# Optimization experiments

Measured on AMD Instinct MI355X. Metric: run time of the kernel, lower is better.

The kernel has to match this reference:

```python
import jax, jax.numpy as jnp
import numpy as np

HIDDEN = 2048
NUM_HEADS = 32
NUM_KV_HEADS = 8
HEAD_DIM = 128
EPS = 1e-6
ROPE_BASE = 10000.0
T = 2048


def setup_inputs() -> dict:
    key = jax.random.key(0)
    k1, k2, k3, k4, k5 = jax.random.split(key, 5)
    q_size = NUM_HEADS * HEAD_DIM
    kv_size = NUM_KV_HEADS * HEAD_DIM
    s = 0.02
    return {
        "positions": jnp.arange(T, dtype=jnp.int32),
        "hidden_states": jax.random.normal(k1, (T, HIDDEN), dtype=jnp.float32),
        "wqkv": jax.random.normal(k2, (q_size + 2 * kv_size, HIDDEN), dtype=jnp.float32) * s,
        "wo": jax.random.normal(k3, (HIDDEN, q_size), dtype=jnp.float32) * s,
        "q_norm_w": jnp.ones((HEAD_DIM,), dtype=jnp.float32),
        "k_norm_w": jnp.ones((HEAD_DIM,), dtype=jnp.float32),
    }


def _rms_norm(x, w, eps=EPS):
    # x: [T, H, D]; normalize over last dim
    var = jnp.mean(jnp.square(x), axis=-1, keepdims=True)
    return x * jax.lax.rsqrt(var + eps) * w


def _rope(positions, x):
    # neox-style rotate-half RoPE. x: [T, H, D]
    half = HEAD_DIM // 2
    inv_freq = 1.0 / (ROPE_BASE ** (jnp.arange(0, half, dtype=jnp.float32) / half))
    ang = positions.astype(jnp.float32)[:, None] * inv_freq  # [T, half]
    cos = jnp.cos(ang)[:, None, :]  # [T, 1, half]
    sin = jnp.sin(ang)[:, None, :]
    x1, x2 = x[..., :half], x[..., half:]
    return jnp.concatenate([x1 * cos - x2 * sin, x2 * cos + x1 * sin], axis=-1)


def reference(positions, hidden_states, wqkv, wo, q_norm_w, k_norm_w):
    q_size = NUM_HEADS * HEAD_DIM
    kv_size = NUM_KV_HEADS * HEAD_DIM
    scaling = HEAD_DIM ** -0.5

    qkv = hidden_states @ wqkv.T  # [T, q_size + 2*kv_size]
    q = qkv[:, :q_size].reshape(-1, NUM_HEADS, HEAD_DIM)
    k = qkv[:, q_size:q_size + kv_size].reshape(-1, NUM_KV_HEADS, HEAD_DIM)
    v = qkv[:, q_size + kv_size:].reshape(-1, NUM_KV_HEADS, HEAD_DIM)

    q = _rms_norm(q, q_norm_w)
    k = _rms_norm(k, k_norm_w)
    q = _rope(positions, q)
    k = _rope(positions, k)

    # GQA: repeat kv heads to match query heads
    group = NUM_HEADS // NUM_KV_HEADS
    k = jnp.repeat(k, group, axis=1)  # [T, H, D]
    v = jnp.repeat(v, group, axis=1)

    scores = jnp.einsum("thd,shd->hts", q, k) * scaling  # [H, T, T]
    causal = positions[:, None] >= positions[None, :]  # [T, T]
    scores = jnp.where(causal[None], scores, jnp.finfo(scores.dtype).min)
    probs = jax.nn.softmax(scores, axis=-1)
    o = jnp.einsum("hts,shd->thd", probs, v)  # [T, H, D]
    return o.reshape(-1, q_size) @ wo.T  # [T, HIDDEN]
```

## Files before the change

### kernel.cpp

```cpp
#include <hip/hip_runtime.h>
#include <hip/hip_bf16.h>

#define T_SEQ   2048
#define HIDDEN  2048
#define NUM_H   32
#define NUM_KV  8
#define HD      128
#define Q_SIZE  4096
#define QKV_N   6144

typedef __bf16 bf16;
typedef __bf16 bf16x8 __attribute__((ext_vector_type(8)));
typedef __bf16 bf16x4 __attribute__((ext_vector_type(4)));
typedef float  floatx4 __attribute__((ext_vector_type(4)));

#define GLOBAL_AS(p) ((const __attribute__((address_space(1))) void*)(p))
#define LDS_AS(p)    ((__attribute__((address_space(3))) void*)(p))

__global__ void detect_dtype(const unsigned short* __restrict__ wq, int* flagp)
{
    const int lane = threadIdx.x;
    int cnt = 0;
    for (int i = lane; i < 512; i += 64) {
        int ef = (wq[i] >> 7) & 0xFF;
        if (ef >= 90 && ef <= 130) cnt++;
    }
    #pragma unroll
    for (int m = 32; m; m >>= 1) cnt += __shfl_xor(cnt, m);
    if (lane == 0) *flagp = (cnt >= 430) ? 1 : 0;
}

__global__ __launch_bounds__(256) void convert_all(
    const void* __restrict__ h, const void* __restrict__ wq,
    const void* __restrict__ wo_, const void* __restrict__ qn,
    const void* __restrict__ kn,
    bf16* __restrict__ hb, bf16* __restrict__ wqb, bf16* __restrict__ wob,
    bf16* __restrict__ qnb, bf16* __restrict__ knb, const int* flagp)
{
    long e = ((long)blockIdx.x * 256 + threadIdx.x) * 8;
    const void* src; bf16* dst; long off;
    if      (e < 4194304)  { src = h;   dst = hb;  off = e; }
    else if (e < 16777216) { src = wq;  dst = wqb; off = e - 4194304; }
    else if (e < 25165824) { src = wo_; dst = wob; off = e - 16777216; }
    else if (e < 25165952) { src = qn;  dst = qnb; off = e - 25165824; }
    else if (e < 25166080) { src = kn;  dst = knb; off = e - 25165952; }
    else return;

    if (*flagp) {
        *(bf16x8*)(dst + off) = *(const bf16x8*)((const bf16*)src + off);
    } else {
        const float* f = (const float*)src + off;
        bf16x8 v;
        #pragma unroll
        for (int i = 0; i < 8; ++i) v[i] = (bf16)f[i];
        *(bf16x8*)(dst + off) = v;
    }
}

__global__ __launch_bounds__(256) void gemm_bt(
    const bf16* __restrict__ A, const bf16* __restrict__ B,
    void* __restrict__ Cv, int M, int N, int K, int lda,
    const int* flagp, int is_final)
{
    __shared__ bf16 As[128 * 32];
    __shared__ bf16 Bs[128 * 32];

    const int tid  = threadIdx.x;
    const int wave = tid >> 6, lane = tid & 63;
    const int quad = lane >> 4, l16 = lane & 15;
    const int wm = (wave & 1) * 64, wn = (wave >> 1) * 64;
    const long baseM = (long)blockIdx.x * 128;
    const long baseN = (long)blockIdx.y * 128;
    const int  bf_out = is_final ? *flagp : 1;

    const int  srow = wave * 16 + (lane >> 2);
    const int  scol = (lane & 3) * 8;
    const long aoff0 = (baseM + srow) * (long)lda + scol;
    const long aoff1 = (baseM + 64 + srow) * (long)lda + scol;
    const long boff0 = (baseN + srow) * (long)K + scol;
    const long boff1 = (baseN + 64 + srow) * (long)K + scol;
    const int  lds0 = wave * 512;
    const int  lds1 = 2048 + wave * 512;

    floatx4 acc[4][4] = {};

    for (int k0 = 0; k0 < K; k0 += 32) {
        __builtin_amdgcn_global_load_lds(GLOBAL_AS(A + aoff0 + k0), LDS_AS(As + lds0), 16, 0, 0);
        __builtin_amdgcn_global_load_lds(GLOBAL_AS(A + aoff1 + k0), LDS_AS(As + lds1), 16, 0, 0);
        __builtin_amdgcn_global_load_lds(GLOBAL_AS(B + boff0 + k0), LDS_AS(Bs + lds0), 16, 0, 0);
        __builtin_amdgcn_global_load_lds(GLOBAL_AS(B + boff1 + k0), LDS_AS(Bs + lds1), 16, 0, 0);
        __syncthreads();

        bf16x8 af[4], bfr[4];
        #pragma unroll
        for (int i = 0; i < 4; ++i)
            af[i] = *(const bf16x8*)(As + (wm + i * 16 + l16) * 32 + quad * 8);
        #pragma unroll
        for (int j = 0; j < 4; ++j)
            bfr[j] = *(const bf16x8*)(Bs + (wn + j * 16 + l16) * 32 + quad * 8);

        #pragma unroll
        for (int i = 0; i < 4; ++i)
            #pragma unroll
            for (int j = 0; j < 4; ++j)
                acc[i][j] = __builtin_amdgcn_mfma_f32_16x16x32_bf16(af[i], bfr[j], acc[i][j], 0, 0, 0);
        __syncthreads();
    }

    #pragma unroll
    for (int i = 0; i < 4; ++i)
        #pragma unroll
        for (int j = 0; j < 4; ++j)
            #pragma unroll
            for (int r = 0; r < 4; ++r) {
                long row = baseM + wm + i * 16 + quad * 4 + r;
                long col = baseN + wn + j * 16 + l16;
                if (bf_out) ((bf16*)Cv)[row * (long)N + col] = (bf16)acc[i][j][r];
                else       ((float*)Cv)[row * (long)N + col] = acc[i][j][r];
            }
}

__global__ __launch_bounds__(256) void gemm_bt64(
    const bf16* __restrict__ A, const bf16* __restrict__ B,
    void* __restrict__ Cv, int M, int N, int K, int lda,
    const int* flagp, int is_final)
{
    __shared__ bf16 As[128 * 32];
    __shared__ bf16 Bs[64 * 32];

    const int tid  = threadIdx.x;
    const int wave = tid >> 6, lane = tid & 63;
    const int quad = lane >> 4, l16 = lane & 15;
    const int wm = (wave & 1) * 64, wn = (wave >> 1) * 32;
    const long baseM = (long)blockIdx.x * 128;
    const long baseN = (long)blockIdx.y * 64;
    const int  bf_out = is_final ? *flagp : 1;

    const int  srow = wave * 16 + (lane >> 2);
    const int  scol = (lane & 3) * 8;
    const long aoff0 = (baseM + srow) * (long)lda + scol;
    const long aoff1 = (baseM + 64 + srow) * (long)lda + scol;
    const long boff0 = (baseN + srow) * (long)K + scol;
    const int  lds0 = wave * 512;
    const int  lds1 = 2048 + wave * 512;

    floatx4 acc[4][2] = {};

    for (int k0 = 0; k0 < K; k0 += 32) {
        __builtin_amdgcn_global_load_lds(GLOBAL_AS(A + aoff0 + k0), LDS_AS(As + lds0), 16, 0, 0);
        __builtin_amdgcn_global_load_lds(GLOBAL_AS(A + aoff1 + k0), LDS_AS(As + lds1), 16, 0, 0);
        __builtin_amdgcn_global_load_lds(GLOBAL_AS(B + boff0 + k0), LDS_AS(Bs + lds0), 16, 0, 0);
        __syncthreads();

        bf16x8 af[4], bfr[2];
        #pragma unroll
        for (int i = 0; i < 4; ++i)
            af[i] = *(const bf16x8*)(As + (wm + i * 16 + l16) * 32 + quad * 8);
        #pragma unroll
        for (int j = 0; j < 2; ++j)
            bfr[j] = *(const bf16x8*)(Bs + (wn + j * 16 + l16) * 32 + quad * 8);

        #pragma unroll
        for (int i = 0; i < 4; ++i)
            #pragma unroll
            for (int j = 0; j < 2; ++j)
                acc[i][j] = __builtin_amdgcn_mfma_f32_16x16x32_bf16(af[i], bfr[j], acc[i][j], 0, 0, 0);
        __syncthreads();
    }

    #pragma unroll
    for (int i = 0; i < 4; ++i)
        #pragma unroll
        for (int j = 0; j < 2; ++j)
            #pragma unroll
            for (int r = 0; r < 4; ++r) {
                long row = baseM + wm + i * 16 + quad * 4 + r;
                long col = baseN + wn + j * 16 + l16;
                if (bf_out) ((bf16*)Cv)[row * (long)N + col] = (bf16)acc[i][j][r];
                else       ((float*)Cv)[row * (long)N + col] = acc[i][j][r];
            }
}

__global__ __launch_bounds__(256) void qkv_post(
    bf16* __restrict__ qkv, const int* __restrict__ positions,
    const bf16* __restrict__ qnw, const bf16* __restrict__ knw)
{
    const int t = blockIdx.x;
    const int tid = threadIdx.x, wave = tid >> 6, lane = tid & 63;
    const float pos = (float)positions[t];

    const float inv = expf(-(float)lane * (float)(9.210340371976184 / 64.0));
    float sn, cs;
    sincosf(pos * inv, &sn, &cs);

    bf16* row = qkv + (long)t * QKV_N;

    for (int u = wave; u < 40; u += 4) {
        bf16* p       = (u < 32) ? row + u * HD : row + Q_SIZE + (u - 32) * HD;
        const bf16* w = (u < 32) ? qnw : knw;
        float x1 = (float)p[lane], x2 = (float)p[lane + 64];
        float ss = x1 * x1 + x2 * x2;
        #pragma unroll
        for (int m = 32; m; m >>= 1) ss += __shfl_xor(ss, m);
        float rr = rsqrtf(ss * (1.f / 128.f) + 1e-6f);
        float y1 = x1 * rr * (float)w[lane];
        float y2 = x2 * rr * (float)w[lane + 64];
        p[lane]      = (bf16)(y1 * cs - y2 * sn);
        p[lane + 64] = (bf16)(y2 * cs + y1 * sn);
    }
}

__global__ __launch_bounds__(256) void vtrans(const bf16* __restrict__ qkv,
                                              bf16* __restrict__ vt)
{
    __shared__ bf16 tile[64][136];
    const int t0 = blockIdx.x * 64, kvh = blockIdx.y, tid = threadIdx.x;

    const int rl = tid >> 4, c8 = (tid & 15) * 8;
    const bf16* src = qkv + (long)t0 * QKV_N + 5120 + kvh * HD;
    #pragma unroll
    for (int it = 0; it < 4; ++it) {
        int r = it * 16 + rl;
        *(bf16x8*)(&tile[r][c8]) = *(const bf16x8*)(src + (long)r * QKV_N + c8);
    }
    __syncthreads();

    const int d = tid >> 1, tb = (tid & 1) * 32;
    bf16* dst = vt + ((long)kvh * HD + d) * T_SEQ + t0 + tb;
    #pragma unroll
    for (int it = 0; it < 4; ++it) {
        bf16x8 v;
        #pragma unroll
        for (int j = 0; j < 8; ++j) v[j] = tile[tb + it * 8 + j][d];
        *(bf16x8*)(dst + it * 8) = v;
    }
}

__global__ __launch_bounds__(256, 3) void attn5(bf16* qkv, const bf16* __restrict__ vt)
{
    __shared__ bf16 Ks[2][64 * 128];
    __shared__ bf16 Vs[128 * 64];

    const int tid  = threadIdx.x, wave = tid >> 6, lane = tid & 63;
    const int quad = lane >> 4, l16 = lane & 15;
    const int h = blockIdx.x, kvh = h >> 2;
    const int iq = 31 - blockIdx.y;
    const int q0 = iq * 64;

    const float C1 = 0.12753236f;
    const float C2 = 17.312340f;

    bf16x8 qf[4];
    {
        const bf16* qa = qkv + (long)(q0 + wave * 16 + l16) * QKV_N + h * HD + quad * 8;
        #pragma unroll
        for (int ks = 0; ks < 4; ++ks) qf[ks] = *(const bf16x8*)(qa + ks * 32);
    }

    floatx4 oacc[8] = {};
    float ls = 0.f;

    const int krl = lane >> 4, kc = lane & 15;
    const int vrl = lane >> 3, vc = lane & 7;
    const int kswz = (kc ^ (wave * 4 + krl)) * 8;
    const int vswz = (vc ^ (vrl & 7)) * 8;
    const int wsig = ((wave & 1) << 1) | (wave >> 1);
    const int sq4  = (((quad & 1) << 1) | (quad >> 1)) << 2;

    const bf16* kg0 = qkv + Q_SIZE + kvh * HD;
    const bf16* vg0 = vt + (long)kvh * HD * T_SEQ;

    auto stageK = [&](int p, int kt) {
        const bf16* kg = kg0 + (long)(kt * 64) * QKV_N;
        #pragma unroll
        for (int it = 0; it < 4; ++it) {
            const int rK = it * 16 + wsig * 4 + krl;
            __builtin_amdgcn_global_load_lds(GLOBAL_AS(kg + (long)rK * QKV_N + kswz),
                                             LDS_AS(&Ks[p][it * 2048 + wave * 512]), 16, 0, 0);
        }
    };
    auto stageV = [&](int kt) {
        const bf16* vg = vg0 + kt * 64;
        #pragma unroll
        for (int it = 0; it < 4; ++it) {
            const int dV = it * 32 + wave * 8 + vrl;
            __builtin_amdgcn_global_load_lds(GLOBAL_AS(vg + (long)dV * T_SEQ + vswz),
                                             LDS_AS(&Vs[it * 2048 + wave * 512]), 16, 0, 0);
        }
    };

    stageK(0, 0);

    const int qg = q0 + wave * 16 + l16;

    for (int kt = 0; kt <= iq; ++kt) {
        const int p = kt & 1;
        __syncthreads();
        stageV(kt);
        if (kt < iq) stageK(p ^ 1, kt + 1);

        const int k0 = kt * 64;

        floatx4 sT[4] = {};
        #pragma unroll
        for (int j2 = 0; j2 < 4; ++j2)
            #pragma unroll
            for (int ks = 0; ks < 4; ++ks) {
                bf16x8 kf = *(const bf16x8*)(&Ks[p][(j2 * 16 + l16) * 128 + (((ks * 4 + quad) ^ l16) * 8)]);
                sT[j2] = __builtin_amdgcn_mfma_f32_16x16x32_bf16(kf, qf[ks], sT[j2], 0, 0, 0);
            }

        const bool diag = (kt == iq);
        unsigned lov[4], hiv[4];
        #pragma unroll
        for (int j2 = 0; j2 < 4; ++j2) {
            float ev[4];
            #pragma unroll
            for (int r = 0; r < 4; ++r) {
                float x = __builtin_amdgcn_exp2f(sT[j2][r] * C1 - C2);
                if (diag && (k0 + j2 * 16 + sq4 + r > qg)) x = 0.f;
                ls += x;
                ev[r] = x;
            }
            asm("v_cvt_pk_bf16_f32 %0, %1, %2" : "=v"(lov[j2]) : "v"(ev[0]), "v"(ev[1]));
            asm("v_cvt_pk_bf16_f32 %0, %1, %2" : "=v"(hiv[j2]) : "v"(ev[2]), "v"(ev[3]));
        }

        bf16x8 pa[2];
        #pragma unroll
        for (int ks2 = 0; ks2 < 2; ++ks2) {
            auto wl = __builtin_amdgcn_permlane32_swap(lov[2 * ks2], lov[2 * ks2 + 1], false, false);
            auto wh = __builtin_amdgcn_permlane32_swap(hiv[2 * ks2], hiv[2 * ks2 + 1], false, false);
            union { unsigned w[4]; bf16x8 v; } u;
            u.w[0] = wl[0]; u.w[1] = wh[0]; u.w[2] = wl[1]; u.w[3] = wh[1];
            pa[ks2] = u.v;
        }

        if (kt < iq) asm volatile("s_waitcnt vmcnt(4)" ::: "memory");
        else         asm volatile("s_waitcnt vmcnt(0)" ::: "memory");
        __builtin_amdgcn_s_barrier();
        __builtin_amdgcn_sched_barrier(0);

        #pragma unroll
        for (int ks2 = 0; ks2 < 2; ++ks2)
            #pragma unroll
            for (int vj = 0; vj < 8; ++vj) {
                const int d = vj * 16 + l16;
                bf16x8 vb = *(const bf16x8*)(&Vs[d * 64 + (((ks2 * 4 + quad) ^ (d & 7)) * 8)]);
                oacc[vj] = __builtin_amdgcn_mfma_f32_16x16x32_bf16(pa[ks2], vb, oacc[vj], 0, 0, 0);
            }
    }

    ls += __shfl_xor(ls, 16); ls += __shfl_xor(ls, 32);
    float rinv[4];
    #pragma unroll
    for (int r = 0; r < 4; ++r) rinv[r] = 1.f / __shfl(ls, quad * 4 + r);

    #pragma unroll
    for (int vj = 0; vj < 8; ++vj)
        #pragma unroll
        for (int r = 0; r < 4; ++r) {
            const long row = q0 + wave * 16 + quad * 4 + r;
            qkv[row * (long)QKV_N + h * HD + vj * 16 + l16] = (bf16)(oacc[vj][r] * rinv[r]);
        }
}

extern "C" void kernel_launch(void* const* d_in, const int* in_sizes, int n_in,
                              void* d_out, int out_size, void* d_ws, size_t ws_size,
                              hipStream_t stream)
{
    const int* positions = (const int*)d_in[0];

    char* ws = (char*)d_ws;
    bf16* qkv  = (bf16*)(ws);
    bf16* hb   = (bf16*)(ws + 25165824);
    bf16* vt   = hb;
    bf16* wqb  = (bf16*)(ws + 33554432);
    bf16* wob  = (bf16*)(ws + 58720256);
    bf16* qnb  = (bf16*)(ws + 75497472);
    bf16* knb  = (bf16*)(ws + 75497728);
    int*  flag = (int*) (ws + 75497984);

    detect_dtype<<<dim3(1), dim3(64), 0, stream>>>((const unsigned short*)d_in[2], flag);
    convert_all<<<dim3(12289), dim3(256), 0, stream>>>(
        d_in[1], d_in[2], d_in[3], d_in[4], d_in[5],
        hb, wqb, wob, qnb, knb, flag);

    dim3 blk(256);
    gemm_bt<<<dim3(T_SEQ / 128, QKV_N / 128), blk, 0, stream>>>(
        hb, wqb, qkv, T_SEQ, QKV_N, HIDDEN, HIDDEN, flag, 0);
    vtrans<<<dim3(T_SEQ / 64, NUM_KV), blk, 0, stream>>>(qkv, vt);
    qkv_post<<<dim3(T_SEQ), blk, 0, stream>>>(qkv, positions, qnb, knb);
    attn5<<<dim3(NUM_H, 32), blk, 0, stream>>>(qkv, vt);
    gemm_bt64<<<dim3(T_SEQ / 128, HIDDEN / 64), blk, 0, stream>>>(
        qkv, wob, d_out, T_SEQ, HIDDEN, Q_SIZE, QKV_N, flag, 1);
}
```

Baseline: 355.4 us.

## Split-K the output projection with a double-buffered 128x128 GEMM and reduce

The output-projection GEMM is rebuilt. Each block now computes a 128x128 tile instead of 128x64, and the LDS tiles are double-buffered so the next K-slice loads while MFMAs run on the current one. K is split in two along grid z, so each half writes fp32 partials to scratch workspace. A new reduce2 kernel sums the two partials and converts to the output dtype. This trades extra partial-sum traffic and one more launch for higher data reuse per block, better load/compute overlap, and the same block count.

```diff
diff --git a/kernel.cpp b/kernel.cpp
--- a/kernel.cpp
+++ b/kernel.cpp
@@ -120,65 +120,97 @@
             }
 }
 
-__global__ __launch_bounds__(256) void gemm_bt64(
+__global__ __launch_bounds__(256) void gemm_db(
     const bf16* __restrict__ A, const bf16* __restrict__ B,
-    void* __restrict__ Cv, int M, int N, int K, int lda,
-    const int* flagp, int is_final)
-{
-    __shared__ bf16 As[128 * 32];
-    __shared__ bf16 Bs[64 * 32];
+    float* __restrict__ Cp, int N, int Kd, int lda, int ldb)
+{
+    __shared__ bf16 As[2][128 * 32];
+    __shared__ bf16 Bs[2][128 * 32];
 
     const int tid  = threadIdx.x;
     const int wave = tid >> 6, lane = tid & 63;
     const int quad = lane >> 4, l16 = lane & 15;
-    const int wm = (wave & 1) * 64, wn = (wave >> 1) * 32;
+    const int wm = (wave & 1) * 64, wn = (wave >> 1) * 64;
     const long baseM = (long)blockIdx.x * 128;
-    const long baseN = (long)blockIdx.y * 64;
-    const int  bf_out = is_final ? *flagp : 1;
+    const long baseN = (long)blockIdx.y * 128;
+    const long koff  = (long)blockIdx.z * Kd;
 
     const int  srow = wave * 16 + (lane >> 2);
     const int  scol = (lane & 3) * 8;
-    const long aoff0 = (baseM + srow) * (long)lda + scol;
-    const long aoff1 = (baseM + 64 + srow) * (long)lda + scol;
-    const long boff0 = (baseN + srow) * (long)K + scol;
+    const long aoff0 = (baseM + srow) * (long)lda + koff + scol;
+    const long aoff1 = (baseM + 64 + srow) * (long)lda + koff + scol;
+    const long boff0 = (baseN + srow) * (long)ldb + koff + scol;
+    const long boff1 = (baseN + 64 + srow) * (long)ldb + koff + scol;
     const int  lds0 = wave * 512;
     const int  lds1 = 2048 + wave * 512;
 
-    floatx4 acc[4][2] = {};
-
-    for (int k0 = 0; k0 < K; k0 += 32) {
-        __builtin_amdgcn_global_load_lds(GLOBAL_AS(A + aoff0 + k0), LDS_AS(As + lds0), 16, 0, 0);
-        __builtin_amdgcn_global_load_lds(GLOBAL_AS(A + aoff1 + k0), LDS_AS(As + lds1), 16, 0, 0);
-        __builtin_amdgcn_global_load_lds(GLOBAL_AS(B + boff0 + k0), LDS_AS(Bs + lds0), 16, 0, 0);
-        __syncthreads();
-
-        bf16x8 af[4], bfr[2];
+    auto stage = [&](int p, int k0) {
+        __builtin_amdgcn_global_load_lds(GLOBAL_AS(A + aoff0 + k0), LDS_AS(As[p] + lds0), 16, 0, 0);
+        __builtin_amdgcn_global_load_lds(GLOBAL_AS(A + aoff1 + k0), LDS_AS(As[p] + lds1), 16, 0, 0);
+        __builtin_amdgcn_global_load_lds(GLOBAL_AS(B + boff0 + k0), LDS_AS(Bs[p] + lds0), 16, 0, 0);
+        __builtin_amdgcn_global_load_lds(GLOBAL_AS(B + boff1 + k0), LDS_AS(Bs[p] + lds1), 16, 0, 0);
+    };
+
+    floatx4 acc[4][4] = {};
+
+    stage(0, 0);
+    asm volatile("s_waitcnt vmcnt(0)" ::: "memory");
+    __builtin_amdgcn_s_barrier();
+
+    int cur = 0;
+    for (int k0 = 0; k0 < Kd; k0 += 32) {
+        if (k0 + 32 < Kd) stage(cur ^ 1, k0 + 32);
+        __builtin_amdgcn_sched_barrier(0);
+
+        bf16x8 af[4], bfr[4];
         #pragma unroll
         for (int i = 0; i < 4; ++i)
-            af[i] = *(const bf16x8*)(As + (wm + i * 16 + l16) * 32 + quad * 8);
-        #pragma unroll
-        for (int j = 0; j < 2; ++j)
-            bfr[j] = *(const bf16x8*)(Bs + (wn + j * 16 + l16) * 32 + quad * 8);
+            af[i] = *(const bf16x8*)(As[cur] + (wm + i * 16 + l16) * 32 + quad * 8);
+        #pragma unroll
+        for (int j = 0; j < 4; ++j)
+            bfr[j] = *(const bf16x8*)(Bs[cur] + (wn + j * 16 + l16) * 32 + quad * 8);
 
         #pragma unroll
         for (int i = 0; i < 4; ++i)
             #pragma unroll
-            for (int j = 0; j < 2; ++j)
+            for (int j = 0; j < 4; ++j)
                 acc[i][j] = __builtin_amdgcn_mfma_f32_16x16x32_bf16(af[i], bfr[j], acc[i][j], 0, 0, 0);
-        __syncthreads();
-    }
-
+
+        asm volatile("s_waitcnt vmcnt(0)" ::: "memory");
+        __builtin_amdgcn_s_barrier();
+        cur ^= 1;
+    }
+
+    const long Mrows = (long)gridDim.x * 128;
+    float* C = Cp + (long)blockIdx.z * Mrows * N;
     #pragma unroll
     for (int i = 0; i < 4; ++i)
         #pragma unroll
-        for (int j = 0; j < 2; ++j)
+        for (int j = 0; j < 4; ++j)
             #pragma unroll
             for (int r = 0; r < 4; ++r) {
                 long row = baseM + wm + i * 16 + quad * 4 + r;
                 long col = baseN + wn + j * 16 + l16;
-                if (bf_out) ((bf16*)Cv)[row * (long)N + col] = (bf16)acc[i][j][r];
-                else       ((float*)Cv)[row * (long)N + col] = acc[i][j][r];
+                C[row * (long)N + col] = acc[i][j][r];
             }
+}
+
+__global__ __launch_bounds__(256) void reduce2(
+    const float* __restrict__ P0, const float* __restrict__ P1,
+    void* __restrict__ out, const int* flagp)
+{
+    long i = ((long)blockIdx.x * 256 + threadIdx.x) * 4;
+    floatx4 a = *(const floatx4*)(P0 + i);
+    floatx4 b = *(const floatx4*)(P1 + i);
+    floatx4 s = a + b;
+    if (*flagp) {
+        bf16x4 o;
+        #pragma unroll
+        for (int r = 0; r < 4; ++r) o[r] = (bf16)s[r];
+        *(bf16x4*)((bf16*)out + i) = o;
+    } else {
+        *(floatx4*)((float*)out + i) = s;
+    }
 }
 
 __global__ __launch_bounds__(256) void qkv_post(
@@ -375,6 +407,8 @@
     bf16* qkv  = (bf16*)(ws);
     bf16* hb   = (bf16*)(ws + 25165824);
     bf16* vt   = hb;
+    float* P0  = (float*)(ws + 25165824);
+    float* P1  = (float*)(ws + 41943040);
     bf16* wqb  = (bf16*)(ws + 33554432);
     bf16* wob  = (bf16*)(ws + 58720256);
     bf16* qnb  = (bf16*)(ws + 75497472);
@@ -392,6 +426,7 @@
     vtrans<<<dim3(T_SEQ / 64, NUM_KV), blk, 0, stream>>>(qkv, vt);
     qkv_post<<<dim3(T_SEQ), blk, 0, stream>>>(qkv, positions, qnb, knb);
     attn5<<<dim3(NUM_H, 32), blk, 0, stream>>>(qkv, vt);
-    gemm_bt64<<<dim3(T_SEQ / 128, HIDDEN / 64), blk, 0, stream>>>(
-        qkv, wob, d_out, T_SEQ, HIDDEN, Q_SIZE, QKV_N, flag, 1);
-}
+    gemm_db<<<dim3(T_SEQ / 128, HIDDEN / 128, 2), blk, 0, stream>>>(
+        qkv, wob, P0, HIDDEN, Q_SIZE / 2, QKV_N, Q_SIZE);
+    reduce2<<<dim3(4096), blk, 0, stream>>>(P0, P1, d_out, flag);
+}
```

Result: faster. 342.3 us (-3.7%).
